# Optimization experiments

Measured on AMD Instinct MI355X. Metric: run time of the kernel, lower is better.

The kernel has to match this reference:

```python
import jax, jax.numpy as jnp
import numpy as np

B, S, D, H = 4, 2048, 1024, 16
HD = D // H


def setup_inputs() -> dict:
    key = jax.random.key(0)
    ks = jax.random.split(key, 5)
    scale = 1.0 / np.sqrt(D)
    return {
        "x": jax.random.normal(ks[0], (B, S, D), dtype=jnp.float32),
        "W_q": jax.random.normal(ks[1], (D, D), dtype=jnp.float32) * scale,
        "W_k": jax.random.normal(ks[2], (D, D), dtype=jnp.float32) * scale,
        "W_v": jax.random.normal(ks[3], (D, D), dtype=jnp.float32) * scale,
        "W_o": jax.random.normal(ks[4], (D, D), dtype=jnp.float32) * scale,
    }


def reference(x, W_q, W_k, W_v, W_o):
    # Linear with weight [out, in]: y = x @ W^T
    def proj(W):
        return jnp.einsum('bsd,ed->bshf', x, W.reshape(H, HD, D).transpose(0, 1, 2).reshape(D, D)) if False else (x @ W.T).reshape(B, S, H, HD).transpose(0, 2, 1, 3)

    q = proj(W_q)  # [B, H, S, HD]
    k = proj(W_k)
    v = proj(W_v)

    scores = jnp.einsum('bhqd,bhkd->bhqk', q, k) / jnp.sqrt(jnp.float32(HD))
    causal = jnp.triu(jnp.ones((S, S), dtype=bool), k=1)  # True above diagonal -> masked
    scores = jnp.where(causal, -jnp.inf, scores)
    probs = jax.nn.softmax(scores, axis=-1)
    out = jnp.einsum('bhqk,bhkd->bhqd', probs, v)  # [B, H, S, HD]
    out = out.transpose(0, 2, 1, 3).reshape(B, S, D)
    return out @ W_o.T
```

## Files before the change

### kernel.cpp

```cpp
#include <hip/hip_runtime.h>
#include <cstdint>
#include <cstddef>

typedef unsigned short u16;
typedef __attribute__((ext_vector_type(8))) short short8;
typedef __attribute__((ext_vector_type(4))) short short4v;
typedef __attribute__((ext_vector_type(8))) unsigned short ushort8v;
typedef __attribute__((ext_vector_type(4))) unsigned short ushort4v;
typedef __attribute__((ext_vector_type(4))) unsigned int uint4v;
typedef __attribute__((ext_vector_type(4))) float f32x4;

#define QSCALE 0.18033688011112042f
#define THR_L2 11.5417f


__device__ __forceinline__ u16 f2bf(float f) {
  unsigned int u = __builtin_bit_cast(unsigned int, f);
  u += 0x7FFFu + ((u >> 16) & 1u);
  return (u16)(u >> 16);
}

__device__ __forceinline__ void async16(const void* g, void* l) {
  __builtin_amdgcn_global_load_lds(
      (const __attribute__((address_space(1))) unsigned int*)g,
      (__attribute__((address_space(3))) unsigned int*)l, 16, 0, 0);
}

__device__ __forceinline__ float fmax3(float a, float b, float c) {
  float r;
  asm("v_max3_f32 %0, %1, %2, %3" : "=v"(r) : "v"(a), "v"(b), "v"(c));
  return r;
}

__device__ __forceinline__ unsigned int cvtpk(float lo, float hi) {
  unsigned int r;
  asm("v_cvt_pk_bf16_f32 %0, %1, %2" : "=v"(r) : "v"(lo), "v"(hi));
  return r;
}


__global__ void cvt_f32_bf16(const float* __restrict__ in, u16* __restrict__ out, int n) {
  int i = (blockIdx.x * 256 + threadIdx.x) * 4;
  if (i >= n) return;
  float4 v = *(const float4*)(in + i);
  ushort4v o;
  o[0] = f2bf(v.x); o[1] = f2bf(v.y); o[2] = f2bf(v.z); o[3] = f2bf(v.w);
  *(ushort4v*)(out + i) = o;
}

__global__ void cvt_w4(const float* __restrict__ a, const float* __restrict__ b,
                       const float* __restrict__ c, const float* __restrict__ d,
                       u16* __restrict__ out) {
  const int i = (blockIdx.x * 256 + threadIdx.x) * 4;
  const float* src = (blockIdx.y == 0) ? a : (blockIdx.y == 1) ? b
                    : (blockIdx.y == 2) ? c : d;
  float4 v = *(const float4*)(src + i);
  ushort4v o;
  o[0] = f2bf(v.x); o[1] = f2bf(v.y); o[2] = f2bf(v.z); o[3] = f2bf(v.w);
  *(ushort4v*)(out + (size_t)blockIdx.y * 1048576 + i) = o;
}


template<int MODE>
__global__ __launch_bounds__(256, 2) void gemm_bt(
    const u16* __restrict__ A, const u16* __restrict__ Bw,
    void* __restrict__ Cout, int M, int N, int K)
{
  const int t = threadIdx.x;
  const int lane = t & 63, w = t >> 6;
  const int li = lane & 15, g = lane >> 4;
  const int wr = w >> 1, wc = w & 1;

  const int nx = gridDim.x;
  const int hwid = blockIdx.y * nx + blockIdx.x;
  const int cpx = (nx * gridDim.y) >> 3;
  const int lid = (hwid & 7) * cpx + (hwid >> 3);
  const int brow = (lid / nx) * 128, bcol = (lid % nx) * 128;

  __shared__ u16 As[128 * 32];
  __shared__ u16 Bs[128 * 32];

  f32x4 acc[4][4];
#pragma unroll
  for (int i = 0; i < 4; ++i)
#pragma unroll
    for (int j = 0; j < 4; ++j) acc[i][j] = f32x4{0.f, 0.f, 0.f, 0.f};

  for (int k0 = 0; k0 < K; k0 += 32) {
#pragma unroll
    for (int L = 0; L < 2; ++L) {
      const int f = t + 256 * L;
      const int row = f >> 2;
      const int cb = ((f & 3) * 16) ^ ((row & 3) << 4);
      async16(A + (size_t)(brow + row) * K + k0 + (cb >> 1),
              &As[(w * 64 + 256 * L) * 8]);
      async16(Bw + (size_t)(bcol + row) * K + k0 + (cb >> 1),
              &Bs[(w * 64 + 256 * L) * 8]);
    }
    __syncthreads();
    short8 af[4], bfr[4];
    const int ksw = (g * 8) ^ ((li & 3) << 3);
#pragma unroll
    for (int mt = 0; mt < 4; ++mt)
      af[mt] = *(const short8*)&As[(wr * 64 + mt * 16 + li) * 32 + ksw];
#pragma unroll
    for (int nt = 0; nt < 4; ++nt)
      bfr[nt] = *(const short8*)&Bs[(wc * 64 + nt * 16 + li) * 32 + ksw];
    __builtin_amdgcn_s_setprio(1);
#pragma unroll
    for (int mt = 0; mt < 4; ++mt)
#pragma unroll
      for (int nt = 0; nt < 4; ++nt)
        acc[mt][nt] = __builtin_amdgcn_mfma_f32_16x16x32_bf16(af[mt], bfr[nt], acc[mt][nt], 0, 0, 0);
    __builtin_amdgcn_s_setprio(0);
    __syncthreads();
  }

#pragma unroll
  for (int mt = 0; mt < 4; ++mt)
#pragma unroll
    for (int nt = 0; nt < 4; ++nt) {
      const int col = bcol + wc * 64 + nt * 16 + li;
#pragma unroll
      for (int r = 0; r < 4; ++r) {
        const int row = brow + wr * 64 + mt * 16 + g * 4 + r;
        float v = acc[mt][nt][r];
        if (MODE == 0) {
          const int which = col >> 10;
          const int c2 = col & 1023;
          if (which == 0) v *= QSCALE;
          const int b = row >> 11, s = row & 2047;
          const int h = c2 >> 6, hd = c2 & 63;
          ((u16*)Cout)[(size_t)which * 8388608 +
                       (((size_t)(b * 16 + h) * 2048) + s) * 64 + hd] = f2bf(v);
        } else {
          ((float*)Cout)[(size_t)row * N + col] = v;
        }
      }
    }
}


__global__ __launch_bounds__(256) void transpose_hd_s(
    const u16* __restrict__ V, u16* __restrict__ VT)
{
  const int sb = blockIdx.x;
  const int bh = blockIdx.y;
  __shared__ u16 tile[64 * 72];
  const int t = threadIdx.x;
  const int r = t >> 3;
  const int c8 = (t & 7) * 8;
  const size_t base = (size_t)bh * 2048 * 64;
#pragma unroll
  for (int half = 0; half < 2; ++half) {
    const int row = r + 32 * half;
    ushort8v v = *(const ushort8v*)(V + base + (size_t)(sb * 64 + row) * 64 + c8);
    *(ushort8v*)&tile[row * 72 + c8] = v;
  }
  __syncthreads();
#pragma unroll
  for (int half = 0; half < 2; ++half) {
    const int hd = r + 32 * half;
    ushort8v o;
#pragma unroll
    for (int j = 0; j < 8; ++j) o[j] = tile[(c8 + j) * 72 + hd];
    *(ushort8v*)(VT + base + (size_t)hd * 2048 + sb * 64 + c8) = o;
  }
}


__global__ __launch_bounds__(256, 2) void flash_attn3(
    const u16* __restrict__ Qp, const u16* __restrict__ Kp,
    const u16* __restrict__ VTp, u16* __restrict__ Oattn)
{
  const int hwid = blockIdx.x;
  const int lid = (hwid & 7) * 64 + (hwid >> 3);
  const int pr = lid & 7, bh = lid >> 3;

  const int t = threadIdx.x;
  const int lane = t & 63, w = t >> 6;
  const int li = lane & 15, g = lane >> 4;

  __shared__ u16 Kl[3][64 * 64];
  __shared__ u16 Vl[3][64 * 64];

  const size_t bh_off = (size_t)bh * (2048 * 64);
  const int tile0 = pr, tile1 = 15 - pr;
  const int njb0 = 2 * tile0 + 2;

  short8 qf0[2][2], qf1[2][2];
#pragma unroll
  for (int qs = 0; qs < 2; ++qs) {
    const u16* qp0 = Qp + bh_off + (size_t)(tile0 * 128 + qs * 64 + w * 16 + li) * 64 + g * 8;
    qf0[qs][0] = *(const short8*)qp0;
    qf0[qs][1] = *(const short8*)(qp0 + 32);
    const u16* qp1 = Qp + bh_off + (size_t)(tile1 * 128 + qs * 64 + w * 16 + li) * 64 + g * 8;
    qf1[qs][0] = *(const short8*)qp1;
    qf1[qs][1] = *(const short8*)(qp1 + 32);
  }
  short8 qc[2][2];
#pragma unroll
  for (int qs = 0; qs < 2; ++qs) { qc[qs][0] = qf0[qs][0]; qc[qs][1] = qf0[qs][1]; }

  int qbase = tile0 * 128;

  f32x4 o_acc[2][4];
#pragma unroll
  for (int qs = 0; qs < 2; ++qs)
#pragma unroll
    for (int i = 0; i < 4; ++i) o_acc[qs][i] = f32x4{0.f, 0.f, 0.f, 0.f};
  float m_i[2] = {-1e30f, -1e30f};
  float l_i[2] = {0.f, 0.f};

  const int b = bh >> 4, h = bh & 15;
  const int ksw = (li & 7) << 3;

  auto STAGE = [&](int i, int s) {
    const int jb = (i < njb0) ? i : (i - njb0);
#pragma unroll
    for (int L = 0; L < 2; ++L) {
      const int f = t + 256 * L;
      const int kbyte = (f * 16) ^ (((f >> 3) & 7) << 4);
      async16(Kp + bh_off + (size_t)jb * 4096 + (kbyte >> 1),
              &Kl[s][(w * 64 + 256 * L) * 8]);
      const int vrow = f >> 3;
      const int vb = ((f & 7) * 16) ^ ((vrow & 7) << 4);
      async16(VTp + bh_off + (size_t)vrow * 2048 + jb * 64 + (vb >> 1),
              &Vl[s][(w * 64 + 256 * L) * 8]);
    }
  };

  auto WRITEO = [&]() {
#pragma unroll
    for (int qs = 0; qs < 2; ++qs) {
      const float inv_l = 1.f / l_i[qs];
      const int qrow = qbase + qs * 64 + w * 16 + li;
      u16* op = Oattn + ((size_t)(b * 2048 + qrow)) * 1024 + h * 64;
#pragma unroll
      for (int dt = 0; dt < 4; ++dt) {
        ushort4v st;
#pragma unroll
        for (int r = 0; r < 4; ++r) st[r] = f2bf(o_acc[qs][dt][r] * inv_l);
        *(ushort4v*)(op + dt * 16 + g * 4) = st;
      }
    }
  };

  STAGE(0, 0);
  STAGE(1, 1);
  asm volatile("s_waitcnt vmcnt(4)" ::: "memory");
  __builtin_amdgcn_s_barrier();

#pragma unroll 1
  for (int i = 0; i < 34; ++i) {
    const int s = i % 3;
    if (i + 2 < 34) STAGE(i + 2, (i + 2) % 3);

    const int jb = (i < njb0) ? i : (i - njb0);
    const u16* __restrict__ Ks = &Kl[s][0];
    const u16* __restrict__ Vs = &Vl[s][0];

    f32x4 s_acc[2][4];
#pragma unroll
    for (int qs = 0; qs < 2; ++qs)
#pragma unroll
      for (int jt = 0; jt < 4; ++jt) s_acc[qs][jt] = f32x4{0.f, 0.f, 0.f, 0.f};
    __builtin_amdgcn_s_setprio(1);
#pragma unroll
    for (int kc = 0; kc < 2; ++kc)
#pragma unroll
      for (int jt = 0; jt < 4; ++jt) {
        short8 kf = *(const short8*)&Ks[(jt * 16 + li) * 64 + ((kc * 32 + g * 8) ^ ksw)];
        s_acc[0][jt] = __builtin_amdgcn_mfma_f32_16x16x32_bf16(kf, qc[0][kc], s_acc[0][jt], 0, 0, 0);
        s_acc[1][jt] = __builtin_amdgcn_mfma_f32_16x16x32_bf16(kf, qc[1][kc], s_acc[1][jt], 0, 0, 0);
      }
    __builtin_amdgcn_s_setprio(0);

    float mx[2];
    bool need = false;
#pragma unroll
    for (int qs = 0; qs < 2; ++qs) {
      if (jb * 64 + 63 > qbase + qs * 64 + w * 16) {
        const int tq = qbase + qs * 64 + w * 16 + li - jb * 64;
#pragma unroll
        for (int jt = 0; jt < 4; ++jt)
#pragma unroll
          for (int r = 0; r < 4; ++r)
            if (jt * 16 + g * 4 + r > tq) s_acc[qs][jt][r] = -1e30f;
      }
      float t0 = fmax3(s_acc[qs][0][0], s_acc[qs][0][1], s_acc[qs][0][2]);
      float t1 = fmax3(s_acc[qs][0][3], s_acc[qs][1][0], s_acc[qs][1][1]);
      float t2 = fmax3(s_acc[qs][1][2], s_acc[qs][1][3], s_acc[qs][2][0]);
      float t3 = fmax3(s_acc[qs][2][1], s_acc[qs][2][2], s_acc[qs][2][3]);
      float t4m = fmax3(s_acc[qs][3][0], s_acc[qs][3][1], s_acc[qs][3][2]);
      float m01 = fmax3(t0, t1, s_acc[qs][3][3]);
      float m23 = fmax3(t2, t3, t4m);
      float mm = fmaxf(m01, m23);
      mm = fmaxf(mm, __shfl_xor(mm, 16));
      mm = fmaxf(mm, __shfl_xor(mm, 32));
      mx[qs] = mm;
      need = need || (mm > m_i[qs] + THR_L2);
    }

    if (__any((int)need)) {
#pragma unroll
      for (int qs = 0; qs < 2; ++qs) {
        const float mn = fmaxf(m_i[qs], mx[qs]);
        const float corr = __builtin_amdgcn_exp2f(m_i[qs] - mn);
        l_i[qs] *= corr;
#pragma unroll
        for (int dt = 0; dt < 4; ++dt) o_acc[qs][dt] *= corr;
        m_i[qs] = mn;
      }
    }

    short8 pf[2][2];
#pragma unroll
    for (int qs = 0; qs < 2; ++qs) {
      const float mi = m_i[qs];
      float ps = 0.f;
#pragma unroll
      for (int jt = 0; jt < 4; ++jt)
#pragma unroll
        for (int r = 0; r < 4; ++r) {
          float e = __builtin_amdgcn_exp2f(s_acc[qs][jt][r] - mi);
          s_acc[qs][jt][r] = e;
          ps += e;
        }
      ps += __shfl_xor(ps, 16);
      ps += __shfl_xor(ps, 32);
      l_i[qs] += ps;
#pragma unroll
      for (int kc = 0; kc < 2; ++kc) {
        uint4v u;
        u[0] = cvtpk(s_acc[qs][2 * kc][0], s_acc[qs][2 * kc][1]);
        u[1] = cvtpk(s_acc[qs][2 * kc][2], s_acc[qs][2 * kc][3]);
        u[2] = cvtpk(s_acc[qs][2 * kc + 1][0], s_acc[qs][2 * kc + 1][1]);
        u[3] = cvtpk(s_acc[qs][2 * kc + 1][2], s_acc[qs][2 * kc + 1][3]);
        pf[qs][kc] = __builtin_bit_cast(short8, u);
      }
    }

    __builtin_amdgcn_s_setprio(1);
#pragma unroll
    for (int kc = 0; kc < 2; ++kc)
#pragma unroll
      for (int dt = 0; dt < 4; ++dt) {
        const int rowb = (dt * 16 + li) * 64;
        short4v v0 = *(const short4v*)&Vs[rowb + ((kc * 32 + g * 4) ^ ksw)];
        short4v v1 = *(const short4v*)&Vs[rowb + ((kc * 32 + 16 + g * 4) ^ ksw)];
        short8 vf = __builtin_shufflevector(v0, v1, 0, 1, 2, 3, 4, 5, 6, 7);
        o_acc[0][dt] = __builtin_amdgcn_mfma_f32_16x16x32_bf16(vf, pf[0][kc], o_acc[0][dt], 0, 0, 0);
        o_acc[1][dt] = __builtin_amdgcn_mfma_f32_16x16x32_bf16(vf, pf[1][kc], o_acc[1][dt], 0, 0, 0);
      }
    __builtin_amdgcn_s_setprio(0);

    asm volatile("s_waitcnt lgkmcnt(0)" ::: "memory");
    if (i < 32) { asm volatile("s_waitcnt vmcnt(4)" ::: "memory"); }
    else        { asm volatile("s_waitcnt vmcnt(0)" ::: "memory"); }
    __builtin_amdgcn_s_barrier();

    if (i == njb0 - 1) {
      WRITEO();
      qbase = tile1 * 128;
#pragma unroll
      for (int qs = 0; qs < 2; ++qs) {
        qc[qs][0] = qf1[qs][0]; qc[qs][1] = qf1[qs][1];
        m_i[qs] = -1e30f; l_i[qs] = 0.f;
#pragma unroll
        for (int dt = 0; dt < 4; ++dt) o_acc[qs][dt] = f32x4{0.f, 0.f, 0.f, 0.f};
      }
    }
  }

  WRITEO();
}


extern "C" void kernel_launch(void* const* d_in, const int* in_sizes, int n_in,
                              void* d_out, int out_size, void* d_ws, size_t ws_size,
                              hipStream_t stream) {
  const float* x  = (const float*)d_in[0];
  const float* Wq = (const float*)d_in[1];
  const float* Wk = (const float*)d_in[2];
  const float* Wv = (const float*)d_in[3];
  const float* Wo = (const float*)d_in[4];

  const size_t NX = 8388608;
  const size_t NW = 1048576;

  u16* xb  = (u16*)d_ws;
  u16* wqb = xb + NX;
  u16* wob = wqb + 3 * NW;
  u16* Qb  = wob + NW;
  u16* Kb  = Qb + NX;
  u16* Vb  = Kb + NX;
  u16* VTb = Vb + NX;
  u16* attnb = Vb;

  cvt_f32_bf16<<<8192, 256, 0, stream>>>(x, xb, (int)NX);
  cvt_w4<<<dim3(1024, 4), 256, 0, stream>>>(Wq, Wk, Wv, Wo, wqb);

  gemm_bt<0><<<dim3(24, 64), 256, 0, stream>>>(xb, wqb, Qb, 8192, 3072, 1024);

  transpose_hd_s<<<dim3(32, 64), 256, 0, stream>>>(Vb, VTb);
  flash_attn3<<<512, 256, 0, stream>>>(Qb, Kb, VTb, attnb);

  gemm_bt<1><<<dim3(8, 64), 256, 0, stream>>>(attnb, wob, d_out, 8192, 1024, 1024);
}
```

Baseline: 183.4 us.

## Pipeline GEMM with 4-stage async LDS ring, 256-row tiles, fused conversion kernel

Rewrites the projection GEMMs to use 512-thread blocks computing 256x128 tiles, with a four-buffer LDS ring that prefetches three K-steps ahead. Explicit vmcnt waits and a single barrier per iteration replace the two __syncthreads. The LDS swizzle is changed to match the new layout. The two fp32-to-bf16 conversion kernels are merged into one launch. The goal is to hide global-load latency behind MFMA work, at the cost of much larger LDS use (96KB) and one block per CU.

```diff
diff --git a/kernel.cpp b/kernel.cpp
--- a/kernel.cpp
+++ b/kernel.cpp
@@ -39,46 +39,49 @@
 }
 
 
-__global__ void cvt_f32_bf16(const float* __restrict__ in, u16* __restrict__ out, int n) {
-  int i = (blockIdx.x * 256 + threadIdx.x) * 4;
-  if (i >= n) return;
-  float4 v = *(const float4*)(in + i);
-  ushort4v o;
-  o[0] = f2bf(v.x); o[1] = f2bf(v.y); o[2] = f2bf(v.z); o[3] = f2bf(v.w);
-  *(ushort4v*)(out + i) = o;
-}
-
-__global__ void cvt_w4(const float* __restrict__ a, const float* __restrict__ b,
-                       const float* __restrict__ c, const float* __restrict__ d,
-                       u16* __restrict__ out) {
-  const int i = (blockIdx.x * 256 + threadIdx.x) * 4;
-  const float* src = (blockIdx.y == 0) ? a : (blockIdx.y == 1) ? b
-                    : (blockIdx.y == 2) ? c : d;
+__global__ void cvt_all(const float* __restrict__ x, const float* __restrict__ Wq,
+                        const float* __restrict__ Wk, const float* __restrict__ Wv,
+                        const float* __restrict__ Wo, u16* __restrict__ out) {
+  const int bid = blockIdx.x;
+  const float* src;
+  int i;
+  size_t doff;
+  if (bid < 8192) {
+    i = bid * 1024 + threadIdx.x * 4;
+    src = x;
+    doff = (size_t)i;
+  } else {
+    const int k = bid - 8192;
+    const int wsel = k >> 10;
+    i = (k & 1023) * 1024 + threadIdx.x * 4;
+    src = (wsel == 0) ? Wq : (wsel == 1) ? Wk : (wsel == 2) ? Wv : Wo;
+    doff = 8388608 + (size_t)wsel * 1048576 + i;
+  }
   float4 v = *(const float4*)(src + i);
   ushort4v o;
   o[0] = f2bf(v.x); o[1] = f2bf(v.y); o[2] = f2bf(v.z); o[3] = f2bf(v.w);
-  *(ushort4v*)(out + (size_t)blockIdx.y * 1048576 + i) = o;
+  *(ushort4v*)(out + doff) = o;
 }
 
 
 template<int MODE>
-__global__ __launch_bounds__(256, 2) void gemm_bt(
+__global__ __launch_bounds__(512, 1) void gemm_qb(
     const u16* __restrict__ A, const u16* __restrict__ Bw,
     void* __restrict__ Cout, int M, int N, int K)
 {
   const int t = threadIdx.x;
   const int lane = t & 63, w = t >> 6;
   const int li = lane & 15, g = lane >> 4;
-  const int wr = w >> 1, wc = w & 1;
+  const int wm = w >> 1, wn = w & 1;
 
   const int nx = gridDim.x;
   const int hwid = blockIdx.y * nx + blockIdx.x;
   const int cpx = (nx * gridDim.y) >> 3;
   const int lid = (hwid & 7) * cpx + (hwid >> 3);
-  const int brow = (lid / nx) * 128, bcol = (lid % nx) * 128;
-
-  __shared__ u16 As[128 * 32];
-  __shared__ u16 Bs[128 * 32];
+  const int brow = (lid / nx) * 256, bcol = (lid % nx) * 128;
+
+  __shared__ u16 As[4][256 * 32];
+  __shared__ u16 Bs[4][128 * 32];
 
   f32x4 acc[4][4];
 #pragma unroll
@@ -86,26 +89,43 @@
 #pragma unroll
     for (int j = 0; j < 4; ++j) acc[i][j] = f32x4{0.f, 0.f, 0.f, 0.f};
 
-  for (int k0 = 0; k0 < K; k0 += 32) {
+  auto STAGE = [&](int T) {
+    const int b = T & 3;
+    const int k0 = T * 32;
 #pragma unroll
     for (int L = 0; L < 2; ++L) {
-      const int f = t + 256 * L;
-      const int row = f >> 2;
-      const int cb = ((f & 3) * 16) ^ ((row & 3) << 4);
-      async16(A + (size_t)(brow + row) * K + k0 + (cb >> 1),
-              &As[(w * 64 + 256 * L) * 8]);
-      async16(Bw + (size_t)(bcol + row) * K + k0 + (cb >> 1),
-              &Bs[(w * 64 + 256 * L) * 8]);
-    }
-    __syncthreads();
+      const int f2 = t + 512 * L;
+      const int row = f2 >> 2;
+      const int cb = ((f2 & 3) * 16) ^ (((row >> 1) & 3) << 4);
+      async16(A + (size_t)(brow + row) * K + k0 + (cb >> 1), &As[b][f2 * 8]);
+    }
+    const int rowb = t >> 2;
+    const int cbb = ((t & 3) * 16) ^ (((rowb >> 1) & 3) << 4);
+    async16(Bw + (size_t)(bcol + rowb) * K + k0 + (cbb >> 1), &Bs[b][t * 8]);
+  };
+
+  STAGE(0); STAGE(1); STAGE(2);
+
+  const int NT = K >> 5;
+  const int ksw = (g * 8) ^ (((li >> 1) & 3) << 3);
+
+#pragma unroll 1
+  for (int T = 0; T < NT; ++T) {
+    if (T < NT - 2)      asm volatile("s_waitcnt vmcnt(6)" ::: "memory");
+    else if (T == NT - 2) asm volatile("s_waitcnt vmcnt(3)" ::: "memory");
+    else                  asm volatile("s_waitcnt vmcnt(0)" ::: "memory");
+    asm volatile("s_barrier" ::: "memory");
+    const int b = T & 3;
     short8 af[4], bfr[4];
-    const int ksw = (g * 8) ^ ((li & 3) << 3);
 #pragma unroll
     for (int mt = 0; mt < 4; ++mt)
-      af[mt] = *(const short8*)&As[(wr * 64 + mt * 16 + li) * 32 + ksw];
+      af[mt] = *(const short8*)&As[b][(wm * 64 + mt * 16 + li) * 32 + ksw];
 #pragma unroll
     for (int nt = 0; nt < 4; ++nt)
-      bfr[nt] = *(const short8*)&Bs[(wc * 64 + nt * 16 + li) * 32 + ksw];
+      bfr[nt] = *(const short8*)&Bs[b][(wn * 64 + nt * 16 + li) * 32 + ksw];
+
+    if (T + 3 < NT) STAGE(T + 3);
+
     __builtin_amdgcn_s_setprio(1);
 #pragma unroll
     for (int mt = 0; mt < 4; ++mt)
@@ -113,26 +133,25 @@
       for (int nt = 0; nt < 4; ++nt)
         acc[mt][nt] = __builtin_amdgcn_mfma_f32_16x16x32_bf16(af[mt], bfr[nt], acc[mt][nt], 0, 0, 0);
     __builtin_amdgcn_s_setprio(0);
-    __syncthreads();
   }
 
 #pragma unroll
   for (int mt = 0; mt < 4; ++mt)
 #pragma unroll
     for (int nt = 0; nt < 4; ++nt) {
-      const int col = bcol + wc * 64 + nt * 16 + li;
+      const int col = bcol + wn * 64 + nt * 16 + li;
 #pragma unroll
       for (int r = 0; r < 4; ++r) {
-        const int row = brow + wr * 64 + mt * 16 + g * 4 + r;
+        const int row = brow + wm * 64 + mt * 16 + g * 4 + r;
         float v = acc[mt][nt][r];
         if (MODE == 0) {
           const int which = col >> 10;
           const int c2 = col & 1023;
           if (which == 0) v *= QSCALE;
-          const int b = row >> 11, s = row & 2047;
+          const int bb = row >> 11, s = row & 2047;
           const int h = c2 >> 6, hd = c2 & 63;
           ((u16*)Cout)[(size_t)which * 8388608 +
-                       (((size_t)(b * 16 + h) * 2048) + s) * 64 + hd] = f2bf(v);
+                       (((size_t)(bb * 16 + h) * 2048) + s) * 64 + hd] = f2bf(v);
         } else {
           ((float*)Cout)[(size_t)row * N + col] = v;
         }
@@ -398,13 +417,12 @@
   u16* VTb = Vb + NX;
   u16* attnb = Vb;
 
-  cvt_f32_bf16<<<8192, 256, 0, stream>>>(x, xb, (int)NX);
-  cvt_w4<<<dim3(1024, 4), 256, 0, stream>>>(Wq, Wk, Wv, Wo, wqb);
-
-  gemm_bt<0><<<dim3(24, 64), 256, 0, stream>>>(xb, wqb, Qb, 8192, 3072, 1024);
+  cvt_all<<<12288, 256, 0, stream>>>(x, Wq, Wk, Wv, Wo, xb);
+
+  gemm_qb<0><<<dim3(24, 32), 512, 0, stream>>>(xb, wqb, Qb, 8192, 3072, 1024);
 
   transpose_hd_s<<<dim3(32, 64), 256, 0, stream>>>(Vb, VTb);
   flash_attn3<<<512, 256, 0, stream>>>(Qb, Kb, VTb, attnb);
 
-  gemm_bt<1><<<dim3(8, 64), 256, 0, stream>>>(attnb, wob, d_out, 8192, 1024, 1024);
-}
+  gemm_qb<1><<<dim3(8, 32), 512, 0, stream>>>(attnb, wob, d_out, 8192, 1024, 1024);
+}
```

After: 176.5 us. 1.04x faster.
